# Optimization experiments

Measured on AMD Instinct MI355X. Metric: run time of the kernel, lower is better.

The kernel has to match this reference:

```python
import jax, jax.numpy as jnp
import numpy as np

INPUT_SIZE = 512
N_THETA = 608  # backcast 512 + forecast 96
N_EXPERTS = 8
TOP_K = 2
LN_EPS = 1e-5


def setup_inputs() -> dict:
    key = jax.random.key(0)
    ks = jax.random.split(key, 5)
    B = 8192
    s = 0.02
    return {
        "insample_y": jax.random.normal(ks[0], (B, INPUT_SIZE), dtype=jnp.float32),
        "ln_gamma": jnp.ones((INPUT_SIZE,), dtype=jnp.float32),
        "ln_beta": jnp.zeros((INPUT_SIZE,), dtype=jnp.float32),
        "Wg": jax.random.normal(ks[1], (INPUT_SIZE, N_EXPERTS), dtype=jnp.float32) * s,
        "W0": jax.random.normal(ks[2], (N_EXPERTS, INPUT_SIZE, 512), dtype=jnp.float32) * s,
        "Wmid": jax.random.normal(ks[3], (3, N_EXPERTS, 512, 512), dtype=jnp.float32) * s,
        "Wout": jax.random.normal(ks[4], (N_EXPERTS, 512, N_THETA), dtype=jnp.float32) * s,
    }


def _layer_norm(x, gamma, beta):
    mu = jnp.mean(x, axis=-1, keepdims=True)
    var = jnp.mean(jnp.square(x - mu), axis=-1, keepdims=True)
    return (x - mu) * jax.lax.rsqrt(var + LN_EPS) * gamma + beta


def reference(insample_y, ln_gamma, ln_beta, Wg, W0, Wmid, Wout):
    x = insample_y  # [B, input_size]
    # Gate: LayerNorm -> Linear(no bias) -> top-k -> softmax over selected logits
    gate_logits = _layer_norm(x, ln_gamma, ln_beta) @ Wg            # [B, E]
    top_vals, top_idx = jax.lax.top_k(gate_logits, TOP_K)           # [B, k]
    gate_w = jax.nn.softmax(top_vals, axis=-1)                      # [B, k]

    # Experts (bias-free MLPs), evaluated densely for all experts
    z = jnp.einsum('bi,eih->beh', x, W0)                            # first linear, no activation
    for l in range(Wmid.shape[0]):
        z = jax.nn.relu(jnp.einsum('beh,eho->beo', z, Wmid[l]))
    theta_all = jnp.einsum('beh,eht->bet', z, Wout)                 # [B, E, n_theta]

    # Combine top-k expert outputs with gate weights
    theta_sel = jnp.take_along_axis(theta_all, top_idx[:, :, None], axis=1)  # [B, k, n_theta]
    theta = jnp.einsum('bk,bkt->bt', gate_w, theta_sel)             # [B, n_theta]

    # Identity basis: split theta into backcast / forecast
    backcast = theta[:, :INPUT_SIZE]
    forecast = theta[:, INPUT_SIZE:]
    return backcast, forecast
```

## Files before the change

### kernel.cpp

```cpp
#include <hip/hip_runtime.h>
#include <hip/hip_bf16.h>
#include <stdint.h>


#define B_ROWS 8192
#define I_DIM  512
#define H_DIM  512
#define E_NUM  8
#define T_DIM  608
#define T_PAD  640
#define CAP    2304
#define TPE    36
#define NT     288
#define NPAD   18432

typedef unsigned short ushort_t;
typedef __attribute__((ext_vector_type(8))) __bf16 bf16x8;
typedef __attribute__((ext_vector_type(8))) unsigned short ushort8;
typedef __attribute__((ext_vector_type(4))) float floatx4;

__device__ __forceinline__ void gload_lds16(const void* g, void* l) {
  __builtin_amdgcn_global_load_lds(
      (const __attribute__((address_space(1))) unsigned int*)g,
      (__attribute__((address_space(3))) unsigned int*)l, 16, 0, 0);
}

__device__ __forceinline__ ushort_t f2bf(float v) {
  __hip_bfloat16 h = __float2bfloat16(v);
  return __builtin_bit_cast(unsigned short, h);
}

__global__ __launch_bounds__(256) void gate_cast_k(
    const float* __restrict__ x, const float* __restrict__ gamma,
    const float* __restrict__ beta, const float* __restrict__ Wg,
    ushort_t* __restrict__ xb, int2* __restrict__ gidx, float2* __restrict__ gw)
{
  const int row  = (blockIdx.x * blockDim.x + threadIdx.x) >> 6;
  const int lane = threadIdx.x & 63;
  const float* xr = x + (size_t)row * I_DIM + lane * 8;
  float4 a = *(const float4*)(xr);
  float4 b = *(const float4*)(xr + 4);
  float xs[8] = {a.x, a.y, a.z, a.w, b.x, b.y, b.z, b.w};

  float s = 0.f;
#pragma unroll
  for (int j = 0; j < 8; ++j) s += xs[j];
#pragma unroll
  for (int off = 32; off; off >>= 1) s += __shfl_xor(s, off);
  const float mu = s * (1.0f / I_DIM);

  float vs = 0.f;
#pragma unroll
  for (int j = 0; j < 8; ++j) { float d = xs[j] - mu; vs += d * d; }
#pragma unroll
  for (int off = 32; off; off >>= 1) vs += __shfl_xor(vs, off);
  const float rstd = rsqrtf(vs * (1.0f / I_DIM) + 1e-5f);

  float lg[8] = {0.f, 0.f, 0.f, 0.f, 0.f, 0.f, 0.f, 0.f};
  const float* gmr = gamma + lane * 8;
  const float* btr = beta + lane * 8;
#pragma unroll
  for (int j = 0; j < 8; ++j) {
    const float y = (xs[j] - mu) * rstd * gmr[j] + btr[j];
    const float* wr = Wg + (size_t)(lane * 8 + j) * E_NUM;
#pragma unroll
    for (int e = 0; e < 8; ++e) lg[e] += y * wr[e];
  }
#pragma unroll
  for (int e = 0; e < 8; ++e)
#pragma unroll
    for (int off = 32; off; off >>= 1) lg[e] += __shfl_xor(lg[e], off);

  ushort8 o;
#pragma unroll
  for (int j = 0; j < 8; ++j) o[j] = f2bf(xs[j]);
  *(ushort8*)(xb + (size_t)row * I_DIM + lane * 8) = o;

  if (lane == 0) {
    int i0 = 0; float b0 = lg[0];
#pragma unroll
    for (int e = 1; e < 8; ++e) if (lg[e] > b0) { b0 = lg[e]; i0 = e; }
    int i1 = -1; float b1 = -3.4e38f;
#pragma unroll
    for (int e = 0; e < 8; ++e) if (e != i0 && lg[e] > b1) { b1 = lg[e]; i1 = e; }
    const float w0 = 1.0f / (1.0f + __expf(b1 - b0));
    gidx[row] = make_int2(i0, i1);
    gw[row] = make_float2(w0, 1.0f - w0);
  }
}

__global__ __launch_bounds__(256) void assign_k(
    const int2* __restrict__ gidx, const float2* __restrict__ gw,
    int* __restrict__ rowmap, float* __restrict__ wmap,
    int* __restrict__ cursor)
{
  __shared__ int lcnt[E_NUM];
  __shared__ int lbase[E_NUM];
  const int tid = threadIdx.x;
  const int row = blockIdx.x * 256 + tid;
  if (tid < E_NUM) lcnt[tid] = 0;
  __syncthreads();
  const int2 g = gidx[row];
  const float2 w = gw[row];
  const int r0 = atomicAdd(&lcnt[g.x], 1);
  const int r1 = atomicAdd(&lcnt[g.y], 1);
  __syncthreads();
  if (tid < E_NUM) lbase[tid] = atomicAdd(&cursor[tid], lcnt[tid]);
  __syncthreads();
  const int p0 = g.x * CAP + lbase[g.x] + r0;
  rowmap[p0] = row; wmap[p0] = w.x;
  const int p1 = g.y * CAP + lbase[g.y] + r1;
  rowmap[p1] = row; wmap[p1] = w.y;
}

__global__ __launch_bounds__(256) void transpose_cast_k(
    const float* __restrict__ src, ushort_t* __restrict__ dst,
    int R, int C, size_t srcBStr, size_t dstBStr)
{
  __shared__ float tile[32][33];
  src += (size_t)blockIdx.z * srcBStr;
  dst += (size_t)blockIdx.z * dstBStr;
  const int c0 = blockIdx.x * 32, r0 = blockIdx.y * 32;
  const int tx = threadIdx.x, ty = threadIdx.y;
#pragma unroll
  for (int i = 0; i < 4; ++i)
    tile[ty + i * 8][tx] = src[(size_t)(r0 + ty + i * 8) * C + c0 + tx];
  __syncthreads();
#pragma unroll
  for (int i = 0; i < 4; ++i) {
    const int c = c0 + ty + i * 8;
    if (c < C) dst[(size_t)c * R + r0 + tx] = f2bf(tile[tx][ty + i * 8]);
  }
}

template <bool GATHER, bool RELU, bool FINAL>
__global__ __launch_bounds__(256) void gemm_k(
    const ushort_t* __restrict__ A,
    const ushort_t* __restrict__ B,
    size_t bEStr,
    const int* __restrict__ rowmap, const float* __restrict__ wmap,
    const int* __restrict__ cursor,
    ushort_t* __restrict__ Z,
    float* __restrict__ out)
{
  constexpr int K = 512;
  __shared__ ushort_t lA[64 * 32];
  __shared__ ushort_t lB[128 * 32];
  __shared__ float wrow[64];
  __shared__ int rrow[64];

  const int t = blockIdx.y;
  const int e = t / TPE;
  if ((t - e * TPE) * 64 >= cursor[e]) return;
  const int zr0 = t * 64;
  const int bn0 = blockIdx.x * 128;

  const int tid = threadIdx.x, wid = tid >> 6, lane = tid & 63;
  const int sr = wid * 16 + (lane >> 2);
  const int sc = (lane & 3) * 8;

  const ushort_t* Bb = B + (size_t)e * bEStr + (size_t)bn0 * K;
  const ushort_t* gb = Bb + (size_t)sr * K + sc;
  const ushort_t* ga;
  if (GATHER) {
    ga = A + (size_t)rowmap[zr0 + sr] * K + sc;
  } else {
    ga = A + (size_t)(zr0 + sr) * K + sc;
  }
  ushort_t* la = lA + wid * 512;
  ushort_t* lb = lB + wid * 512;

  floatx4 acc[2][4] = {};
  const int wm = (wid >> 1) * 32, wn = (wid & 1) * 64;
  const int fr = lane & 15, q = lane >> 4;

  for (int k0 = 0; k0 < K; k0 += 32) {
    gload_lds16(ga + k0, la);
    gload_lds16(gb + k0, lb);
    gload_lds16(gb + (size_t)64 * K + k0, lb + 64 * 32);
    __syncthreads();

    bf16x8 af[2], bfr[4];
#pragma unroll
    for (int mi = 0; mi < 2; ++mi)
      af[mi] = *(const bf16x8*)(lA + (wm + mi * 16 + fr) * 32 + q * 8);
#pragma unroll
    for (int ni = 0; ni < 4; ++ni)
      bfr[ni] = *(const bf16x8*)(lB + (wn + ni * 16 + fr) * 32 + q * 8);
#pragma unroll
    for (int mi = 0; mi < 2; ++mi)
#pragma unroll
      for (int ni = 0; ni < 4; ++ni)
        acc[mi][ni] = __builtin_amdgcn_mfma_f32_16x16x32_bf16(
            af[mi], bfr[ni], acc[mi][ni], 0, 0, 0);
    __syncthreads();
  }

  if (!FINAL) {
    ushort_t* Zb = Z + (size_t)zr0 * H_DIM + bn0;
#pragma unroll
    for (int mi = 0; mi < 2; ++mi)
#pragma unroll
      for (int r = 0; r < 4; ++r) {
        const int row = wm + mi * 16 + q * 4 + r;
        ushort_t* zr = Zb + (size_t)row * H_DIM + wn + fr;
#pragma unroll
        for (int ni = 0; ni < 4; ++ni) {
          float v = acc[mi][ni][r];
          if (RELU) v = fmaxf(v, 0.0f);
          zr[ni * 16] = f2bf(v);
        }
      }
  } else {
    if (tid < 64) {
      wrow[tid] = wmap[zr0 + tid];
      rrow[tid] = rowmap[zr0 + tid];
    }
    __syncthreads();
#pragma unroll
    for (int mi = 0; mi < 2; ++mi)
#pragma unroll
      for (int r = 0; r < 4; ++r) {
        const int row = wm + mi * 16 + q * 4 + r;
        const float w = wrow[row];
        if (w != 0.0f) {
          const size_t orig = rrow[row];
#pragma unroll
          for (int ni = 0; ni < 4; ++ni) {
            const int col = bn0 + wn + ni * 16 + fr;
            if (col < T_DIM) {
              const float v = acc[mi][ni][r] * w;
              float* dst = (col < I_DIM)
                  ? out + orig * I_DIM + col
                  : out + (size_t)B_ROWS * I_DIM + orig * (T_DIM - I_DIM) +
                        (col - I_DIM);
              atomicAdd(dst, v);
            }
          }
        }
      }
  }
}

extern "C" void kernel_launch(void* const* d_in, const int* in_sizes, int n_in,
                              void* d_out, int out_size, void* d_ws,
                              size_t ws_size, hipStream_t stream) {
  const float* x     = (const float*)d_in[0];
  const float* gamma = (const float*)d_in[1];
  const float* beta  = (const float*)d_in[2];
  const float* Wg    = (const float*)d_in[3];
  const float* W0    = (const float*)d_in[4];
  const float* Wmid  = (const float*)d_in[5];
  const float* Wout  = (const float*)d_in[6];
  float* out = (float*)d_out;

  char* ws = (char*)d_ws;
  size_t off = 0;
  auto alloc = [&](size_t bytes) -> char* {
    char* p = ws + off;
    off += (bytes + 255) & ~(size_t)255;
    return p;
  };

  const size_t SQ = (size_t)H_DIM * H_DIM;
  ushort_t* xb    = (ushort_t*)alloc((size_t)B_ROWS * I_DIM * 2);
  ushort_t* W0t   = (ushort_t*)alloc((size_t)E_NUM * SQ * 2);
  ushort_t* Wmidt = (ushort_t*)alloc((size_t)3 * E_NUM * SQ * 2);
  ushort_t* Woutt = (ushort_t*)alloc((size_t)E_NUM * T_PAD * H_DIM * 2);
  int2*   gidx  = (int2*)alloc((size_t)B_ROWS * sizeof(int2));
  float2* gwv   = (float2*)alloc((size_t)B_ROWS * sizeof(float2));
  int*   rmap   = (int*)alloc(NPAD * sizeof(int));
  float* wmap   = (float*)alloc(NPAD * sizeof(float));
  int*   cursor = (int*)alloc(E_NUM * sizeof(int));
  ushort_t* z0 = (ushort_t*)alloc((size_t)NPAD * H_DIM * 2);
  ushort_t* z1 = (ushort_t*)alloc((size_t)NPAD * H_DIM * 2);

  hipMemsetAsync(d_out, 0, (size_t)out_size * sizeof(float), stream);
  hipMemsetAsync(rmap, 0, NPAD * sizeof(int), stream);
  hipMemsetAsync(wmap, 0, NPAD * sizeof(float), stream);
  hipMemsetAsync(cursor, 0, E_NUM * sizeof(int), stream);

  gate_cast_k<<<dim3(B_ROWS / 4), 256, 0, stream>>>(x, gamma, beta, Wg, xb,
                                                    gidx, gwv);
  transpose_cast_k<<<dim3(16, 16, 8), dim3(32, 8), 0, stream>>>(
      W0, W0t, 512, 512, SQ, SQ);
  transpose_cast_k<<<dim3(16, 16, 24), dim3(32, 8), 0, stream>>>(
      Wmid, Wmidt, 512, 512, SQ, SQ);
  transpose_cast_k<<<dim3(19, 16, 8), dim3(32, 8), 0, stream>>>(
      Wout, Woutt, 512, 608, (size_t)512 * 608, (size_t)T_PAD * 512);
  assign_k<<<dim3(B_ROWS / 256), 256, 0, stream>>>(gidx, gwv, rmap, wmap,
                                                   cursor);

  const dim3 gmid(H_DIM / 128, NT);
  const dim3 gfin(T_PAD / 128, NT);
  gemm_k<true, false, false><<<gmid, 256, 0, stream>>>(
      xb, W0t, SQ, rmap, wmap, cursor, z0, nullptr);
  gemm_k<false, true, false><<<gmid, 256, 0, stream>>>(
      z0, Wmidt + 0 * E_NUM * SQ, SQ, rmap, wmap, cursor, z1, nullptr);
  gemm_k<false, true, false><<<gmid, 256, 0, stream>>>(
      z1, Wmidt + 1 * E_NUM * SQ, SQ, rmap, wmap, cursor, z0, nullptr);
  gemm_k<false, true, false><<<gmid, 256, 0, stream>>>(
      z0, Wmidt + 2 * E_NUM * SQ, SQ, rmap, wmap, cursor, z1, nullptr);
  gemm_k<false, false, true><<<gfin, 256, 0, stream>>>(
      z1, Woutt, (size_t)T_PAD * H_DIM, rmap, wmap, cursor, nullptr, out);
}
```

Baseline: 288.8 us.

## Fuse all five expert GEMM layers into one kernel keeping activations in LDS

Replaces the five separate per-layer GEMM launches with a single fused kernel. Each 32-row tile gathers its input rows into LDS, runs all four hidden layers with the activation kept resident in LDS, then does the output projection with atomic accumulation. This removes the global round trips for intermediate activations and four kernel launches. In exchange each block streams the full weight matrices and owns all columns, which gives fewer blocks (576 vs 288x4 tiles), less parallelism per layer, and weight loads that are not double-buffered.

```diff
diff --git a/kernel.cpp b/kernel.cpp
--- a/kernel.cpp
+++ b/kernel.cpp
@@ -9,10 +9,12 @@
 #define E_NUM  8
 #define T_DIM  608
 #define T_PAD  640
+#define BM     32
 #define CAP    2304
-#define TPE    36
-#define NT     288
+#define TPE    72
+#define NT     576
 #define NPAD   18432
+#define ZSTR   520
 
 typedef unsigned short ushort_t;
 typedef __attribute__((ext_vector_type(8))) __bf16 bf16x8;
@@ -133,101 +135,128 @@
   }
 }
 
-template <bool GATHER, bool RELU, bool FINAL>
-__global__ __launch_bounds__(256) void gemm_k(
-    const ushort_t* __restrict__ A,
-    const ushort_t* __restrict__ B,
-    size_t bEStr,
+__global__ __launch_bounds__(256) void moe_fused_k(
+    const ushort_t* __restrict__ xb,
+    const ushort_t* __restrict__ W0t,
+    const ushort_t* __restrict__ Wmidt,
+    const ushort_t* __restrict__ Woutt,
     const int* __restrict__ rowmap, const float* __restrict__ wmap,
-    const int* __restrict__ cursor,
-    ushort_t* __restrict__ Z,
-    float* __restrict__ out)
+    const int* __restrict__ cursor, float* __restrict__ out)
 {
-  constexpr int K = 512;
-  __shared__ ushort_t lA[64 * 32];
-  __shared__ ushort_t lB[128 * 32];
-  __shared__ float wrow[64];
-  __shared__ int rrow[64];
-
-  const int t = blockIdx.y;
+  __shared__ ushort_t zt[BM * ZSTR];
+  __shared__ ushort_t lB[T_PAD * 32];
+  __shared__ int rrow[BM];
+  __shared__ float wrow[BM];
+
+  const int t = blockIdx.x;
   const int e = t / TPE;
-  if ((t - e * TPE) * 64 >= cursor[e]) return;
-  const int zr0 = t * 64;
-  const int bn0 = blockIdx.x * 128;
+  if ((t - e * TPE) * BM >= cursor[e]) return;
+  const int zr0 = t * BM;
 
   const int tid = threadIdx.x, wid = tid >> 6, lane = tid & 63;
-  const int sr = wid * 16 + (lane >> 2);
-  const int sc = (lane & 3) * 8;
-
-  const ushort_t* Bb = B + (size_t)e * bEStr + (size_t)bn0 * K;
-  const ushort_t* gb = Bb + (size_t)sr * K + sc;
-  const ushort_t* ga;
-  if (GATHER) {
-    ga = A + (size_t)rowmap[zr0 + sr] * K + sc;
-  } else {
-    ga = A + (size_t)(zr0 + sr) * K + sc;
-  }
-  ushort_t* la = lA + wid * 512;
-  ushort_t* lb = lB + wid * 512;
-
-  floatx4 acc[2][4] = {};
-  const int wm = (wid >> 1) * 32, wn = (wid & 1) * 64;
   const int fr = lane & 15, q = lane >> 4;
 
-  for (int k0 = 0; k0 < K; k0 += 32) {
-    gload_lds16(ga + k0, la);
-    gload_lds16(gb + k0, lb);
-    gload_lds16(gb + (size_t)64 * K + k0, lb + 64 * 32);
+  if (tid < BM) {
+    rrow[tid] = rowmap[zr0 + tid];
+    wrow[tid] = wmap[zr0 + tid];
+  }
+  __syncthreads();
+
+#pragma unroll
+  for (int i = 0; i < 8; ++i) {
+    const int r = wid * 8 + i;
+    gload_lds16(xb + (size_t)rrow[r] * I_DIM + lane * 8, zt + r * ZSTR);
+  }
+
+  const size_t SQ = (size_t)512 * 512;
+  const ushort_t* W0p = W0t + (size_t)e * SQ;
+  const ushort_t* Wm0 = Wmidt + (size_t)(0 * E_NUM + e) * SQ;
+  const ushort_t* Wm1 = Wmidt + (size_t)(1 * E_NUM + e) * SQ;
+  const ushort_t* Wm2 = Wmidt + (size_t)(2 * E_NUM + e) * SQ;
+
+  for (int l = 0; l < 4; ++l) {
+    const ushort_t* W = (l == 0) ? W0p : (l == 1) ? Wm0 : (l == 2) ? Wm1 : Wm2;
+    const int wn = wid * 128;
+    floatx4 acc[2][8] = {};
+    for (int k0 = 0; k0 < 512; k0 += 32) {
+#pragma unroll
+      for (int i = 0; i < 8; ++i) {
+        const int rb = wid * 128 + i * 16;
+        gload_lds16(W + (size_t)(rb + (lane >> 2)) * 512 + k0 + (lane & 3) * 8,
+                    lB + rb * 32);
+      }
+      __syncthreads();
+      bf16x8 af[2], bf[8];
+#pragma unroll
+      for (int mi = 0; mi < 2; ++mi)
+        af[mi] = *(const bf16x8*)(zt + (mi * 16 + fr) * ZSTR + k0 + q * 8);
+#pragma unroll
+      for (int ni = 0; ni < 8; ++ni)
+        bf[ni] = *(const bf16x8*)(lB + (wn + ni * 16 + fr) * 32 + q * 8);
+#pragma unroll
+      for (int mi = 0; mi < 2; ++mi)
+#pragma unroll
+        for (int ni = 0; ni < 8; ++ni)
+          acc[mi][ni] = __builtin_amdgcn_mfma_f32_16x16x32_bf16(
+              af[mi], bf[ni], acc[mi][ni], 0, 0, 0);
+      __syncthreads();
+    }
+#pragma unroll
+    for (int mi = 0; mi < 2; ++mi)
+#pragma unroll
+      for (int ni = 0; ni < 8; ++ni)
+#pragma unroll
+        for (int r = 0; r < 4; ++r) {
+          float v = acc[mi][ni][r];
+          if (l > 0) v = fmaxf(v, 0.0f);
+          const unsigned int b = f2bf(v);
+          const unsigned int nb = (unsigned int)__shfl_xor((int)b, 1);
+          if (!(lane & 1)) {
+            *(unsigned int*)(zt + (mi * 16 + q * 4 + r) * ZSTR + wn + ni * 16 +
+                             fr) = b | (nb << 16);
+          }
+        }
     __syncthreads();
-
-    bf16x8 af[2], bfr[4];
+  }
+
+  {
+    const ushort_t* W = Woutt + (size_t)e * T_PAD * 512;
+    const int wn = wid * 160;
+    floatx4 acc[2][10] = {};
+    for (int k0 = 0; k0 < 512; k0 += 32) {
+#pragma unroll
+      for (int i = 0; i < 10; ++i) {
+        const int rb = wid * 160 + i * 16;
+        gload_lds16(W + (size_t)(rb + (lane >> 2)) * 512 + k0 + (lane & 3) * 8,
+                    lB + rb * 32);
+      }
+      __syncthreads();
+      bf16x8 af[2], bf[10];
+#pragma unroll
+      for (int mi = 0; mi < 2; ++mi)
+        af[mi] = *(const bf16x8*)(zt + (mi * 16 + fr) * ZSTR + k0 + q * 8);
+#pragma unroll
+      for (int ni = 0; ni < 10; ++ni)
+        bf[ni] = *(const bf16x8*)(lB + (wn + ni * 16 + fr) * 32 + q * 8);
+#pragma unroll
+      for (int mi = 0; mi < 2; ++mi)
+#pragma unroll
+        for (int ni = 0; ni < 10; ++ni)
+          acc[mi][ni] = __builtin_amdgcn_mfma_f32_16x16x32_bf16(
+              af[mi], bf[ni], acc[mi][ni], 0, 0, 0);
+      __syncthreads();
+    }
 #pragma unroll
     for (int mi = 0; mi < 2; ++mi)
-      af[mi] = *(const bf16x8*)(lA + (wm + mi * 16 + fr) * 32 + q * 8);
-#pragma unroll
-    for (int ni = 0; ni < 4; ++ni)
-      bfr[ni] = *(const bf16x8*)(lB + (wn + ni * 16 + fr) * 32 + q * 8);
-#pragma unroll
-    for (int mi = 0; mi < 2; ++mi)
-#pragma unroll
-      for (int ni = 0; ni < 4; ++ni)
-        acc[mi][ni] = __builtin_amdgcn_mfma_f32_16x16x32_bf16(
-            af[mi], bfr[ni], acc[mi][ni], 0, 0, 0);
-    __syncthreads();
-  }
-
-  if (!FINAL) {
-    ushort_t* Zb = Z + (size_t)zr0 * H_DIM + bn0;
-#pragma unroll
-    for (int mi = 0; mi < 2; ++mi)
 #pragma unroll
       for (int r = 0; r < 4; ++r) {
-        const int row = wm + mi * 16 + q * 4 + r;
-        ushort_t* zr = Zb + (size_t)row * H_DIM + wn + fr;
-#pragma unroll
-        for (int ni = 0; ni < 4; ++ni) {
-          float v = acc[mi][ni][r];
-          if (RELU) v = fmaxf(v, 0.0f);
-          zr[ni * 16] = f2bf(v);
-        }
-      }
-  } else {
-    if (tid < 64) {
-      wrow[tid] = wmap[zr0 + tid];
-      rrow[tid] = rowmap[zr0 + tid];
-    }
-    __syncthreads();
-#pragma unroll
-    for (int mi = 0; mi < 2; ++mi)
-#pragma unroll
-      for (int r = 0; r < 4; ++r) {
-        const int row = wm + mi * 16 + q * 4 + r;
+        const int row = mi * 16 + q * 4 + r;
         const float w = wrow[row];
         if (w != 0.0f) {
-          const size_t orig = rrow[row];
-#pragma unroll
-          for (int ni = 0; ni < 4; ++ni) {
-            const int col = bn0 + wn + ni * 16 + fr;
+          const size_t orig = (size_t)rrow[row];
+#pragma unroll
+          for (int ni = 0; ni < 10; ++ni) {
+            const int col = wn + ni * 16 + fr;
             if (col < T_DIM) {
               const float v = acc[mi][ni][r] * w;
               float* dst = (col < I_DIM)
@@ -272,8 +301,6 @@
   int*   rmap   = (int*)alloc(NPAD * sizeof(int));
   float* wmap   = (float*)alloc(NPAD * sizeof(float));
   int*   cursor = (int*)alloc(E_NUM * sizeof(int));
-  ushort_t* z0 = (ushort_t*)alloc((size_t)NPAD * H_DIM * 2);
-  ushort_t* z1 = (ushort_t*)alloc((size_t)NPAD * H_DIM * 2);
 
   hipMemsetAsync(d_out, 0, (size_t)out_size * sizeof(float), stream);
   hipMemsetAsync(rmap, 0, NPAD * sizeof(int), stream);
@@ -291,16 +318,6 @@
   assign_k<<<dim3(B_ROWS / 256), 256, 0, stream>>>(gidx, gwv, rmap, wmap,
                                                    cursor);
 
-  const dim3 gmid(H_DIM / 128, NT);
-  const dim3 gfin(T_PAD / 128, NT);
-  gemm_k<true, false, false><<<gmid, 256, 0, stream>>>(
-      xb, W0t, SQ, rmap, wmap, cursor, z0, nullptr);
-  gemm_k<false, true, false><<<gmid, 256, 0, stream>>>(
-      z0, Wmidt + 0 * E_NUM * SQ, SQ, rmap, wmap, cursor, z1, nullptr);
-  gemm_k<false, true, false><<<gmid, 256, 0, stream>>>(
-      z1, Wmidt + 1 * E_NUM * SQ, SQ, rmap, wmap, cursor, z0, nullptr);
-  gemm_k<false, true, false><<<gmid, 256, 0, stream>>>(
-      z0, Wmidt + 2 * E_NUM * SQ, SQ, rmap, wmap, cursor, z1, nullptr);
-  gemm_k<false, false, true><<<gfin, 256, 0, stream>>>(
-      z1, Woutt, (size_t)T_PAD * H_DIM, rmap, wmap, cursor, nullptr, out);
-}
+  moe_fused_k<<<dim3(NT), 256, 0, stream>>>(xb, W0t, Wmidt, Woutt, rmap, wmap,
+                                            cursor, out);
+}
```

Result: slower. 330.3 us (+14.4%).

## Pre-swizzle weights and activations into MFMA fragment layout, drop LDS staging

Applied to the files above, without the earlier changes.

Weights are now cast into a layout where each 16-column, 32-k chunk matches the per-lane MFMA fragment order. Intermediate activations are also written in that swizzled layout, so the GEMM can load bf16x8 fragments straight from global memory into registers with no LDS staging and no __syncthreads. The GEMM becomes a single-wave 64x64 tile per block with a fully unrolled K loop. This removes LDS traffic and barriers, but it loses cross-wave data sharing, relies on cache for reuse, and the gather path reads A rows directly.

```diff
diff --git a/kernel.cpp b/kernel.cpp
--- a/kernel.cpp
+++ b/kernel.cpp
@@ -18,12 +18,6 @@
 typedef __attribute__((ext_vector_type(8))) __bf16 bf16x8;
 typedef __attribute__((ext_vector_type(8))) unsigned short ushort8;
 typedef __attribute__((ext_vector_type(4))) float floatx4;
-
-__device__ __forceinline__ void gload_lds16(const void* g, void* l) {
-  __builtin_amdgcn_global_load_lds(
-      (const __attribute__((address_space(1))) unsigned int*)g,
-      (__attribute__((address_space(3))) unsigned int*)l, 16, 0, 0);
-}
 
 __device__ __forceinline__ ushort_t f2bf(float v) {
   __hip_bfloat16 h = __float2bfloat16(v);
@@ -113,121 +107,113 @@
   rowmap[p1] = row; wmap[p1] = w.y;
 }
 
-__global__ __launch_bounds__(256) void transpose_cast_k(
+__global__ __launch_bounds__(256) void swz_weights_k(
     const float* __restrict__ src, ushort_t* __restrict__ dst,
-    int R, int C, size_t srcBStr, size_t dstBStr)
-{
-  __shared__ float tile[32][33];
-  src += (size_t)blockIdx.z * srcBStr;
-  dst += (size_t)blockIdx.z * dstBStr;
-  const int c0 = blockIdx.x * 32, r0 = blockIdx.y * 32;
-  const int tx = threadIdx.x, ty = threadIdx.y;
-#pragma unroll
-  for (int i = 0; i < 4; ++i)
-    tile[ty + i * 8][tx] = src[(size_t)(r0 + ty + i * 8) * C + c0 + tx];
-  __syncthreads();
-#pragma unroll
-  for (int i = 0; i < 4; ++i) {
-    const int c = c0 + ty + i * 8;
-    if (c < C) dst[(size_t)c * R + r0 + tx] = f2bf(tile[tx][ty + i * 8]);
-  }
+    int N, size_t srcZStr)
+{
+  const int jcount = gridDim.x;
+  const int j = blockIdx.x;
+  const int c = blockIdx.y * 4 + (threadIdx.x >> 6);
+  const int z = blockIdx.z;
+  const int lane = threadIdx.x & 63;
+  const int fr = lane & 15, q = lane >> 4;
+  const int n = j * 16 + fr;
+  const float* s = src + (size_t)z * srcZStr;
+  ushort8 o;
+#pragma unroll
+  for (int u = 0; u < 8; ++u) {
+    const int k = c * 32 + q * 8 + u;
+    o[u] = (n < N) ? f2bf(s[(size_t)k * N + n]) : (ushort_t)0;
+  }
+  *(ushort8*)(dst + ((size_t)(z * jcount + j) * 16 + c) * 512 + lane * 8) = o;
 }
 
 template <bool GATHER, bool RELU, bool FINAL>
-__global__ __launch_bounds__(256) void gemm_k(
+__global__ __launch_bounds__(64) void gemm_k(
     const ushort_t* __restrict__ A,
     const ushort_t* __restrict__ B,
-    size_t bEStr,
+    int NJB,
     const int* __restrict__ rowmap, const float* __restrict__ wmap,
     const int* __restrict__ cursor,
     ushort_t* __restrict__ Z,
     float* __restrict__ out)
 {
-  constexpr int K = 512;
-  __shared__ ushort_t lA[64 * 32];
-  __shared__ ushort_t lB[128 * 32];
-  __shared__ float wrow[64];
-  __shared__ int rrow[64];
-
   const int t = blockIdx.y;
   const int e = t / TPE;
   if ((t - e * TPE) * 64 >= cursor[e]) return;
   const int zr0 = t * 64;
-  const int bn0 = blockIdx.x * 128;
-
-  const int tid = threadIdx.x, wid = tid >> 6, lane = tid & 63;
-  const int sr = wid * 16 + (lane >> 2);
-  const int sc = (lane & 3) * 8;
-
-  const ushort_t* Bb = B + (size_t)e * bEStr + (size_t)bn0 * K;
-  const ushort_t* gb = Bb + (size_t)sr * K + sc;
-  const ushort_t* ga;
+  const int bn0 = blockIdx.x * 64;
+
+  const int lane = threadIdx.x;
+  const int fr = lane & 15, q = lane >> 4;
+
+  const ushort_t* Bb =
+      B + ((size_t)e * NJB + (bn0 >> 4)) * (16 * 512) + lane * 8;
+
+  const ushort_t *a0, *a1, *a2, *a3;
   if (GATHER) {
-    ga = A + (size_t)rowmap[zr0 + sr] * K + sc;
+    a0 = A + (size_t)rowmap[zr0 + 0 * 16 + fr] * 512 + q * 8;
+    a1 = A + (size_t)rowmap[zr0 + 1 * 16 + fr] * 512 + q * 8;
+    a2 = A + (size_t)rowmap[zr0 + 2 * 16 + fr] * 512 + q * 8;
+    a3 = A + (size_t)rowmap[zr0 + 3 * 16 + fr] * 512 + q * 8;
   } else {
-    ga = A + (size_t)(zr0 + sr) * K + sc;
-  }
-  ushort_t* la = lA + wid * 512;
-  ushort_t* lb = lB + wid * 512;
-
-  floatx4 acc[2][4] = {};
-  const int wm = (wid >> 1) * 32, wn = (wid & 1) * 64;
-  const int fr = lane & 15, q = lane >> 4;
-
-  for (int k0 = 0; k0 < K; k0 += 32) {
-    gload_lds16(ga + k0, la);
-    gload_lds16(gb + k0, lb);
-    gload_lds16(gb + (size_t)64 * K + k0, lb + 64 * 32);
-    __syncthreads();
-
-    bf16x8 af[2], bfr[4];
-#pragma unroll
-    for (int mi = 0; mi < 2; ++mi)
-      af[mi] = *(const bf16x8*)(lA + (wm + mi * 16 + fr) * 32 + q * 8);
+    const ushort_t* Az = A + (size_t)(zr0 >> 4) * (16 * 512) + lane * 8;
+    a0 = Az + 0 * 16 * 512;
+    a1 = Az + 1 * 16 * 512;
+    a2 = Az + 2 * 16 * 512;
+    a3 = Az + 3 * 16 * 512;
+  }
+
+  floatx4 acc[4][4] = {};
+
+#pragma unroll
+  for (int c = 0; c < 16; ++c) {
+    const int ao = GATHER ? c * 32 : c * 512;
+    bf16x8 af[4], bf[4];
+    af[0] = *(const bf16x8*)(a0 + ao);
+    af[1] = *(const bf16x8*)(a1 + ao);
+    af[2] = *(const bf16x8*)(a2 + ao);
+    af[3] = *(const bf16x8*)(a3 + ao);
 #pragma unroll
     for (int ni = 0; ni < 4; ++ni)
-      bfr[ni] = *(const bf16x8*)(lB + (wn + ni * 16 + fr) * 32 + q * 8);
-#pragma unroll
-    for (int mi = 0; mi < 2; ++mi)
+      bf[ni] = *(const bf16x8*)(Bb + (ni * 16 + c) * 512);
+#pragma unroll
+    for (int mi = 0; mi < 4; ++mi)
 #pragma unroll
       for (int ni = 0; ni < 4; ++ni)
         acc[mi][ni] = __builtin_amdgcn_mfma_f32_16x16x32_bf16(
-            af[mi], bfr[ni], acc[mi][ni], 0, 0, 0);
-    __syncthreads();
+            af[mi], bf[ni], acc[mi][ni], 0, 0, 0);
   }
 
   if (!FINAL) {
-    ushort_t* Zb = Z + (size_t)zr0 * H_DIM + bn0;
-#pragma unroll
-    for (int mi = 0; mi < 2; ++mi)
-#pragma unroll
-      for (int r = 0; r < 4; ++r) {
-        const int row = wm + mi * 16 + q * 4 + r;
-        ushort_t* zr = Zb + (size_t)row * H_DIM + wn + fr;
-#pragma unroll
-        for (int ni = 0; ni < 4; ++ni) {
+#pragma unroll
+    for (int mi = 0; mi < 4; ++mi) {
+      const size_t jbase = (size_t)((zr0 >> 4) + mi) * 16;
+#pragma unroll
+      for (int ni = 0; ni < 4; ++ni) {
+        const int n = bn0 + ni * 16 + fr;
+        const int cK = n >> 5, qK = (n >> 3) & 3, uK = n & 7;
+#pragma unroll
+        for (int r = 0; r < 4; ++r) {
           float v = acc[mi][ni][r];
           if (RELU) v = fmaxf(v, 0.0f);
-          zr[ni * 16] = f2bf(v);
+          const int mf = q * 4 + r;
+          Z[(jbase + cK) * 512 + (qK * 16 + mf) * 8 + uK] = f2bf(v);
         }
       }
+    }
   } else {
-    if (tid < 64) {
-      wrow[tid] = wmap[zr0 + tid];
-      rrow[tid] = rowmap[zr0 + tid];
-    }
-    __syncthreads();
-#pragma unroll
-    for (int mi = 0; mi < 2; ++mi)
+#pragma unroll
+    for (int mi = 0; mi < 4; ++mi)
 #pragma unroll
       for (int r = 0; r < 4; ++r) {
-        const int row = wm + mi * 16 + q * 4 + r;
-        const float w = wrow[row];
+        const int row = zr0 + mi * 16 + q * 4 + r;
+        const float w = wmap[row];
         if (w != 0.0f) {
-          const size_t orig = rrow[row];
+          const size_t orig = (size_t)rowmap[row];
 #pragma unroll
           for (int ni = 0; ni < 4; ++ni) {
-            const int col = bn0 + wn + ni * 16 + fr;
+            const int col = bn0 + ni * 16 + fr;
             if (col < T_DIM) {
               const float v = acc[mi][ni][r] * w;
               float* dst = (col < I_DIM)
@@ -282,25 +268,23 @@
 
   gate_cast_k<<<dim3(B_ROWS / 4), 256, 0, stream>>>(x, gamma, beta, Wg, xb,
                                                     gidx, gwv);
-  transpose_cast_k<<<dim3(16, 16, 8), dim3(32, 8), 0, stream>>>(
-      W0, W0t, 512, 512, SQ, SQ);
-  transpose_cast_k<<<dim3(16, 16, 24), dim3(32, 8), 0, stream>>>(
-      Wmid, Wmidt, 512, 512, SQ, SQ);
-  transpose_cast_k<<<dim3(19, 16, 8), dim3(32, 8), 0, stream>>>(
-      Wout, Woutt, 512, 608, (size_t)512 * 608, (size_t)T_PAD * 512);
+  swz_weights_k<<<dim3(32, 4, 8), 256, 0, stream>>>(W0, W0t, 512, SQ);
+  swz_weights_k<<<dim3(32, 4, 24), 256, 0, stream>>>(Wmid, Wmidt, 512, SQ);
+  swz_weights_k<<<dim3(40, 4, 8), 256, 0, stream>>>(Wout, Woutt, 608,
+                                                    (size_t)512 * 608);
   assign_k<<<dim3(B_ROWS / 256), 256, 0, stream>>>(gidx, gwv, rmap, wmap,
                                                    cursor);
 
-  const dim3 gmid(H_DIM / 128, NT);
-  const dim3 gfin(T_PAD / 128, NT);
-  gemm_k<true, false, false><<<gmid, 256, 0, stream>>>(
-      xb, W0t, SQ, rmap, wmap, cursor, z0, nullptr);
-  gemm_k<false, true, false><<<gmid, 256, 0, stream>>>(
-      z0, Wmidt + 0 * E_NUM * SQ, SQ, rmap, wmap, cursor, z1, nullptr);
-  gemm_k<false, true, false><<<gmid, 256, 0, stream>>>(
-      z1, Wmidt + 1 * E_NUM * SQ, SQ, rmap, wmap, cursor, z0, nullptr);
-  gemm_k<false, true, false><<<gmid, 256, 0, stream>>>(
-      z0, Wmidt + 2 * E_NUM * SQ, SQ, rmap, wmap, cursor, z1, nullptr);
-  gemm_k<false, false, true><<<gfin, 256, 0, stream>>>(
-      z1, Woutt, (size_t)T_PAD * H_DIM, rmap, wmap, cursor, nullptr, out);
-}
+  const dim3 gmid(H_DIM / 64, NT);
+  const dim3 gfin(T_PAD / 64, NT);
+  gemm_k<true, false, false><<<gmid, 64, 0, stream>>>(
+      xb, W0t, 32, rmap, wmap, cursor, z0, nullptr);
+  gemm_k<false, true, false><<<gmid, 64, 0, stream>>>(
+      z0, Wmidt + 0 * E_NUM * SQ, 32, rmap, wmap, cursor, z1, nullptr);
+  gemm_k<false, true, false><<<gmid, 64, 0, stream>>>(
+      z1, Wmidt + 1 * E_NUM * SQ, 32, rmap, wmap, cursor, z0, nullptr);
+  gemm_k<false, true, false><<<gmid, 64, 0, stream>>>(
+      z0, Wmidt + 2 * E_NUM * SQ, 32, rmap, wmap, cursor, z1, nullptr);
+  gemm_k<false, false, true><<<gfin, 64, 0, stream>>>(
+      z1, Woutt, 40, rmap, wmap, cursor, nullptr, out);
+}
```

Result: slower. 350.2 us (+21.3%).
